# Performance work log

Measured on AMD Instinct MI355X. Metric: run time of the kernel, lower is better.

## Reference

```python
import jax, jax.numpy as jnp
import numpy as np

# ---- static hash-grid config (instant-NGP style, matches tcnn hash.json) ----
N_LEVELS = 16
F_PER_LEVEL = 2
LOG2_T = 19
TABLE_SIZE = 2 ** LOG2_T          # 524288 entries per level
BASE_RES = 16
PER_LEVEL_SCALE = 1.3819          # finest res ~2048
RES = [int(np.floor(BASE_RES * PER_LEVEL_SCALE ** l)) for l in range(N_LEVELS)]
N_POINTS = 2 ** 21
PRIME_Y = np.uint32(2654435761)   # tcnn spatial-hash prime

_CORNERS = jnp.array([[0, 0], [1, 0], [0, 1], [1, 1]], dtype=jnp.uint32)


def _level_features(x, table, res):
    """Bilinear hash-grid lookup for one level. x: [N,2] in [0,1). -> [N,F]."""
    pos = x * res                      # [N,2]
    x0f = jnp.floor(pos)
    w = pos - x0f                      # interpolation fractions [N,2]
    x0 = x0f.astype(jnp.uint32)
    c = x0[:, None, :] + _CORNERS[None]            # [N,4,2] corner coords
    if (res + 1) ** 2 <= TABLE_SIZE:
        # dense grid fits in the table: linear indexing (as tcnn does)
        idx = c[..., 0] + c[..., 1] * jnp.uint32(res + 1)
    else:
        # spatial hash with uint32 wraparound
        idx = (c[..., 0] ^ (c[..., 1] * PRIME_Y)) & jnp.uint32(TABLE_SIZE - 1)
    feats = table[idx.astype(jnp.int32)]           # [N,4,F] irregular gather
    wx = jnp.where(_CORNERS[None, :, 0] == 1, w[:, None, 0], 1.0 - w[:, None, 0])
    wy = jnp.where(_CORNERS[None, :, 1] == 1, w[:, None, 1], 1.0 - w[:, None, 1])
    return jnp.sum(feats * (wx * wy)[..., None], axis=1)  # [N,F]


def setup_inputs() -> dict:
    key = jax.random.key(0)
    k1, k2, k3, k4, k5 = jax.random.split(key, 5)
    x = jax.random.uniform(k1, (N_POINTS, 2), dtype=jnp.float32)
    # tcnn hash tables are initialized uniform in [-1e-4, 1e-4]
    tables = jax.random.uniform(k2, (N_LEVELS, TABLE_SIZE, F_PER_LEVEL),
                                dtype=jnp.float32, minval=-1e-4, maxval=1e-4)
    d_in = 2 + N_LEVELS * F_PER_LEVEL  # 34
    h = 64
    w1 = jax.random.normal(k3, (d_in, h), dtype=jnp.float32) * (1.0 / np.sqrt(d_in))
    w2 = jax.random.normal(k4, (h, h), dtype=jnp.float32) * (1.0 / np.sqrt(h))
    w3 = jax.random.normal(k5, (h, 3), dtype=jnp.float32) * (1.0 / np.sqrt(h))
    return {"x": x, "tables": tables, "w1": w1, "w2": w2, "w3": w3}


def reference(x, tables, w1, w2, w3):
    # multi-res hash grid encode (16 levels, static small loop)
    feats = [_level_features(x, tables[l], RES[l]) for l in range(N_LEVELS)]
    enc = jnp.concatenate([x] + feats, axis=1)     # [N, 2 + 32]
    # tiny fused MLP decode (no biases, as in tcnn networks)
    h = jax.nn.relu(enc @ w1)
    h = jax.nn.relu(h @ w2)
    return h @ w3                                   # [N, 3]
```

## Files before the change

### kernel.cpp

```cpp
#include <hip/hip_runtime.h>

typedef unsigned int u32;
typedef unsigned short u16;
typedef __attribute__((ext_vector_type(8))) short s16x8;
typedef __attribute__((ext_vector_type(4))) float f32x4;
typedef float f32x4a __attribute__((ext_vector_type(4), aligned(8)));
typedef u32  u32x2a  __attribute__((ext_vector_type(2), aligned(4)));

#define TBL    524288u
#define TMASK  (TBL - 1u)
#define HPRIME 2654435761u

__device__ constexpr int RESI[16] = {16,22,30,42,58,80,111,153,212,294,406,561,775,1072,1481,2047};

static __device__ __forceinline__ u16 f2bf(float f){
  u32 u = __builtin_bit_cast(u32, f);
  return (u16)((u + 0x7fffu + ((u >> 16) & 1u)) >> 16);
}
static __device__ __forceinline__ float bf2f(u16 h){ return __builtin_bit_cast(float, (u32)h << 16); }
static __device__ __forceinline__ float blo(u32 e){ return __builtin_bit_cast(float, (u32)(e << 16)); }
static __device__ __forceinline__ float bhi(u32 e){ return __builtin_bit_cast(float, (u32)(e & 0xffff0000u)); }
static __device__ __forceinline__ u32 packbf2(float a, float b){ return (u32)f2bf(a) | ((u32)f2bf(b) << 16); }
static __device__ __forceinline__ u32 cvtpk(float a, float b){
  u32 r; asm("v_cvt_pk_bf16_f32 %0, %1, %2" : "=v"(r) : "v"(a), "v"(b)); return r;
}

#define MFMA(A,B,C) __builtin_amdgcn_mfma_f32_16x16x32_bf16((A),(B),(C),0,0,0)

__global__ __launch_bounds__(256) void cvt_tab(const float4* __restrict__ src,
                                               uint2* __restrict__ dst, int n4) {
  for (int i = blockIdx.x*256 + threadIdx.x; i < n4; i += gridDim.x*256) {
    const float4 v = src[i];
    dst[i] = make_uint2(packbf2(v.x, v.y), packbf2(v.z, v.w));
  }
}

template<bool PACKED>
__global__ __launch_bounds__(256, 2) void ngp_fused(
    const float2* __restrict__ xq,
    const float2* __restrict__ tab32,
    const u32*    __restrict__ ctab,
    const float*  __restrict__ w1,
    const float*  __restrict__ w2,
    const float*  __restrict__ w3,
    float* __restrict__ out,
    int iters)
{
  __shared__ __align__(16) u16   encS[256 * 40];
  __shared__ __align__(16) float xyS [256 * 2];
  __shared__ __align__(16) u16   hS  [4][2][16*80];
  __shared__ __align__(16) s16x8 wS  [10][64];

  const int tid  = threadIdx.x;
  const int lane = tid & 63;
  const int wv   = tid >> 6;
  const int m    = lane & 15;
  const int q    = lane >> 4;

  float w1x[4], w1y[4];
  s16x8 B1[4], B2h[4][2], B3h[2];
  #pragma unroll
  for (int c = 0; c < 4; ++c) {
    const int n = c*16 + m;
    w1x[c] = w1[n]; w1y[c] = w1[64 + n];
    s16x8 f1;
    #pragma unroll
    for (int j = 0; j < 8; ++j) {
      const int k = q*8 + j;
      f1[j] = (short)f2bf(w1[(2 + k)*64 + n]);
    }
    B1[c] = f1;
    #pragma unroll
    for (int s = 0; s < 2; ++s) {
      s16x8 fh, fl;
      #pragma unroll
      for (int j = 0; j < 8; ++j) {
        const int k = s*32 + q*8 + j;
        const float v = w2[k*64 + n];
        const u16 h = f2bf(v);
        fh[j] = (short)h; fl[j] = (short)f2bf(v - bf2f(h));
      }
      B2h[c][s] = fh;
      if (wv == 0) wS[c*2 + s][lane] = fl;
    }
  }
  #pragma unroll
  for (int s = 0; s < 2; ++s) {
    s16x8 fh, fl;
    #pragma unroll
    for (int j = 0; j < 8; ++j) {
      const int k = s*32 + q*8 + j;
      const float v = (m < 3) ? w3[k*3 + m] : 0.f;
      const u16 h = f2bf(v);
      fh[j] = (short)h; fl[j] = (short)f2bf(v - bf2f(h));
    }
    B3h[s] = fh;
    if (wv == 0) wS[8 + s][lane] = fl;
  }
  __syncthreads();

  u16* const hpl = &hS[wv][0][0];
  u16* const lpl = &hS[wv][1][0];
  const int mq8  = (m & 12) << 1;

  for (int it = 0; it < iters; ++it) {
    const int base = (blockIdx.x * iters + it) << 8;

    {
      const float2 xy = xq[base + tid];
      ((float2*)xyS)[tid] = xy;
      const float xf = xy.x, yf = xy.y;
      u32 er[16];
      if constexpr (PACKED) {
        u32 hv[4][4];
        #pragma unroll
        for (int l = 12; l < 16; ++l) {
          const int res = RESI[l];
          const u32 ix = (u32)floorf(xf * (float)res);
          const u32 iy = (u32)floorf(yf * (float)res);
          const u32 hy = iy * HPRIME, hy1 = hy + HPRIME;
          const u32* t = ctab + (size_t)l * TBL;
          hv[l-12][0] = t[( ix       ^ hy ) & TMASK];
          hv[l-12][1] = t[((ix + 1u) ^ hy ) & TMASK];
          hv[l-12][2] = t[( ix       ^ hy1) & TMASK];
          hv[l-12][3] = t[((ix + 1u) ^ hy1) & TMASK];
        }
        #pragma unroll
        for (int l = 0; l < 12; ++l) {
          const int res = RESI[l];
          const float px = xf * (float)res, py = yf * (float)res;
          const float fx = floorf(px), fy = floorf(py);
          const float wx = px - fx, wy = py - fy;
          const u32 ix = (u32)fx, iy = (u32)fy;
          const float w00 = (1.f-wx)*(1.f-wy), w10 = wx*(1.f-wy);
          const float w01 = (1.f-wx)*wy,       w11 = wx*wy;
          const u32 st  = (u32)res + 1u;
          const u32 i00 = ix + iy*st;
          const u32* t = ctab + (size_t)l * TBL;
          const u32x2a eA = *(const u32x2a*)&t[i00];
          const u32x2a eB = *(const u32x2a*)&t[i00 + st];
          const float f0 = blo(eA[0])*w00 + blo(eA[1])*w10 + blo(eB[0])*w01 + blo(eB[1])*w11;
          const float f1 = bhi(eA[0])*w00 + bhi(eA[1])*w10 + bhi(eB[0])*w01 + bhi(eB[1])*w11;
          er[l] = cvtpk(f0, f1);
        }
        #pragma unroll
        for (int hl = 0; hl < 4; ++hl) {
          const int res = RESI[12 + hl];
          const float px = xf * (float)res, py = yf * (float)res;
          const float wx = px - floorf(px), wy = py - floorf(py);
          const float w00 = (1.f-wx)*(1.f-wy), w10 = wx*(1.f-wy);
          const float w01 = (1.f-wx)*wy,       w11 = wx*wy;
          const float f0 = blo(hv[hl][0])*w00 + blo(hv[hl][1])*w10
                         + blo(hv[hl][2])*w01 + blo(hv[hl][3])*w11;
          const float f1 = bhi(hv[hl][0])*w00 + bhi(hv[hl][1])*w10
                         + bhi(hv[hl][2])*w01 + bhi(hv[hl][3])*w11;
          er[12 + hl] = cvtpk(f0, f1);
        }
      } else {
        #pragma unroll
        for (int l = 0; l < 16; ++l) {
          const int res = RESI[l];
          const float px = xf * (float)res, py = yf * (float)res;
          const float fx = floorf(px), fy = floorf(py);
          const float wx = px - fx, wy = py - fy;
          const u32 ix = (u32)fx, iy = (u32)fy;
          const float w00 = (1.f-wx)*(1.f-wy), w10 = wx*(1.f-wy);
          const float w01 = (1.f-wx)*wy,       w11 = wx*wy;
          float f0, f1;
          if (l < 12) {
            const u32 st  = (u32)res + 1u;
            const u32 i00 = ix + iy*st;
            const float2* t = tab32 + (size_t)l * TBL;
            const f32x4a eA = *(const f32x4a*)&t[i00];
            const f32x4a eB = *(const f32x4a*)&t[i00 + st];
            f0 = eA[0]*w00 + eA[2]*w10 + eB[0]*w01 + eB[2]*w11;
            f1 = eA[1]*w00 + eA[3]*w10 + eB[1]*w01 + eB[3]*w11;
          } else {
            const u32 hy = iy * HPRIME, hy1 = hy + HPRIME;
            const u32 i00 = ( ix        ^ hy ) & TMASK;
            const u32 i10 = ((ix + 1u)  ^ hy ) & TMASK;
            const u32 i01 = ( ix        ^ hy1) & TMASK;
            const u32 i11 = ((ix + 1u)  ^ hy1) & TMASK;
            const float2* t = tab32 + (size_t)l * TBL;
            const float2 e00 = t[i00], e10 = t[i10], e01 = t[i01], e11 = t[i11];
            f0 = e00.x*w00 + e10.x*w10 + e01.x*w01 + e11.x*w11;
            f1 = e00.y*w00 + e10.y*w10 + e01.y*w01 + e11.y*w11;
          }
          er[l] = cvtpk(f0, f1);
        }
      }
      uint4* rowp = (uint4*)&encS[tid * 40];
      rowp[0] = make_uint4(er[0],  er[1],  er[2],  er[3]);
      rowp[1] = make_uint4(er[4],  er[5],  er[6],  er[7]);
      rowp[2] = make_uint4(er[8],  er[9],  er[10], er[11]);
      rowp[3] = make_uint4(er[12], er[13], er[14], er[15]);
    }

    #pragma unroll 1
    for (int t4 = 0; t4 < 4; ++t4) {
      const int rbase = wv*64 + t4*16;
      const s16x8 a1 = *(const s16x8*)&encS[(rbase + m)*40 + q*8];

      float xr[4], yr[4];
      #pragma unroll
      for (int r = 0; r < 4; ++r) {
        const float2 v = ((const float2*)xyS)[rbase + q*4 + r];
        xr[r] = v.x; yr[r] = v.y;
      }

      f32x4 acc[4];
      #pragma unroll
      for (int c = 0; c < 4; ++c) {
        f32x4 z;
        #pragma unroll
        for (int r = 0; r < 4; ++r) z[r] = xr[r]*w1x[c] + yr[r]*w1y[c];
        acc[c] = MFMA(a1, B1[c], z);
      }

      #pragma unroll
      for (int c = 0; c < 4; ++c)
        #pragma unroll
        for (int r = 0; r < 4; ++r) {
          const float h = fmaxf(acc[c][r], 0.f);
          const u32 hp_ = cvtpk(h, h);
          const float lf = h - __builtin_bit_cast(float, hp_ << 16);
          const u32 lp_ = cvtpk(lf, lf);
          const int idx = (q*4 + r)*80 + ((c*16 + m) ^ (q << 3));
          hpl[idx] = (u16)hp_;
          lpl[idx] = (u16)lp_;
        }

      s16x8 hi0 = *(const s16x8*)&hpl[m*80 + ((q*8) ^ mq8)];
      s16x8 hi1 = *(const s16x8*)&hpl[m*80 + 32 + ((q*8) ^ mq8)];
      s16x8 lo0 = *(const s16x8*)&lpl[m*80 + ((q*8) ^ mq8)];
      s16x8 lo1 = *(const s16x8*)&lpl[m*80 + 32 + ((q*8) ^ mq8)];

      #pragma unroll
      for (int c = 0; c < 4; ++c) {
        const s16x8 b2l0 = wS[c*2 + 0][lane];
        const s16x8 b2l1 = wS[c*2 + 1][lane];
        f32x4 z = {0.f,0.f,0.f,0.f};
        z = MFMA(hi0, B2h[c][0], z); z = MFMA(hi1, B2h[c][1], z);
        z = MFMA(lo0, B2h[c][0], z); z = MFMA(lo1, B2h[c][1], z);
        z = MFMA(hi0, b2l0,      z); z = MFMA(hi1, b2l1,      z);
        acc[c] = z;
      }

      #pragma unroll
      for (int c = 0; c < 4; ++c)
        #pragma unroll
        for (int r = 0; r < 4; ++r) {
          const float h = fmaxf(acc[c][r], 0.f);
          const u32 hp_ = cvtpk(h, h);
          const float lf = h - __builtin_bit_cast(float, hp_ << 16);
          const u32 lp_ = cvtpk(lf, lf);
          const int idx = (q*4 + r)*80 + ((c*16 + m) ^ (q << 3));
          hpl[idx] = (u16)hp_;
          lpl[idx] = (u16)lp_;
        }

      hi0 = *(const s16x8*)&hpl[m*80 + ((q*8) ^ mq8)];
      hi1 = *(const s16x8*)&hpl[m*80 + 32 + ((q*8) ^ mq8)];
      lo0 = *(const s16x8*)&lpl[m*80 + ((q*8) ^ mq8)];
      lo1 = *(const s16x8*)&lpl[m*80 + 32 + ((q*8) ^ mq8)];

      const s16x8 b3l0 = wS[8][lane];
      const s16x8 b3l1 = wS[9][lane];
      f32x4 z = {0.f,0.f,0.f,0.f};
      z = MFMA(hi0, B3h[0], z); z = MFMA(hi1, B3h[1], z);
      z = MFMA(lo0, B3h[0], z); z = MFMA(lo1, B3h[1], z);
      z = MFMA(hi0, b3l0,   z); z = MFMA(hi1, b3l1,   z);

      if (m < 3) {
        #pragma unroll
        for (int r = 0; r < 4; ++r)
          out[(size_t)(base + rbase + q*4 + r)*3 + m] = z[r];
      }
    }
  }
}

extern "C" void kernel_launch(void* const* d_in, const int* in_sizes, int n_in,
                              void* d_out, int out_size, void* d_ws, size_t ws_size,
                              hipStream_t stream) {
  const int N = in_sizes[0] / 2;
  const int ITERS = 4;
  const int blocks = N / (256 * ITERS);
  const size_t ctab_bytes = (size_t)16 * TBL * 4;
  if (ws_size >= ctab_bytes) {
    cvt_tab<<<2048, 256, 0, stream>>>((const float4*)d_in[1], (uint2*)d_ws, (int)(16*TBL/2));
    ngp_fused<true><<<blocks, 256, 0, stream>>>(
        (const float2*)d_in[0], (const float2*)d_in[1], (const u32*)d_ws,
        (const float*)d_in[2], (const float*)d_in[3], (const float*)d_in[4],
        (float*)d_out, ITERS);
  } else {
    ngp_fused<false><<<blocks, 256, 0, stream>>>(
        (const float2*)d_in[0], (const float2*)d_in[1], (const u32*)d_ws,
        (const float*)d_in[2], (const float*)d_in[3], (const float*)d_in[4],
        (float*)d_out, ITERS);
  }
}
```

Before: 433.7 us.

## Sort points by Morton key before hash-grid lookup and scatter outputs

Adds a counting sort of input points into a 256x256 Morton-ordered bin layout (histogram, scan, scatter kernels), so the fused encoder+MLP kernel processes spatially coherent points and its table gathers get better cache locality. Outputs are written back through a permutation array. It also changes the LDS hidden-activation layout from an XOR-swizzled 80-stride to a plain 72-stride padding. The cost is extra kernels with global atomics, a single-block scan, and extra workspace and memory traffic, and the new padding may change bank conflicts.

```diff
diff --git a/kernel.cpp b/kernel.cpp
--- a/kernel.cpp
+++ b/kernel.cpp
@@ -10,6 +10,7 @@
 #define TBL    524288u
 #define TMASK  (TBL - 1u)
 #define HPRIME 2654435761u
+#define NBINS  65536
 
 __device__ constexpr int RESI[16] = {16,22,30,42,58,80,111,153,212,294,406,561,775,1072,1481,2047};
 
@@ -24,6 +25,18 @@
 static __device__ __forceinline__ u32 cvtpk(float a, float b){
   u32 r; asm("v_cvt_pk_bf16_f32 %0, %1, %2" : "=v"(r) : "v"(a), "v"(b)); return r;
 }
+static __device__ __forceinline__ u32 spread8(u32 v){
+  v &= 0xFFu;
+  v = (v | (v << 4)) & 0x0F0Fu;
+  v = (v | (v << 2)) & 0x3333u;
+  v = (v | (v << 1)) & 0x5555u;
+  return v;
+}
+static __device__ __forceinline__ u32 mkey(float x, float y){
+  u32 kx = (u32)(x * 256.f); kx = kx > 255u ? 255u : kx;
+  u32 ky = (u32)(y * 256.f); ky = ky > 255u ? 255u : ky;
+  return spread8(kx) | (spread8(ky) << 1);
+}
 
 #define MFMA(A,B,C) __builtin_amdgcn_mfma_f32_16x16x32_bf16((A),(B),(C),0,0,0)
 
@@ -35,11 +48,51 @@
   }
 }
 
-template<bool PACKED>
+__global__ __launch_bounds__(256) void hist_k(const float2* __restrict__ xq,
+                                              u32* __restrict__ hist, int n) {
+  for (int i = blockIdx.x*256 + threadIdx.x; i < n; i += gridDim.x*256) {
+    const float2 p = xq[i];
+    atomicAdd(&hist[mkey(p.x, p.y)], 1u);
+  }
+}
+__global__ __launch_bounds__(1024) void scan_k(u32* __restrict__ hist) {
+  __shared__ u32 part[1024];
+  const int t = threadIdx.x;
+  u32 s = 0;
+  for (int i = 0; i < 64; ++i) s += hist[t*64 + i];
+  part[t] = s;
+  __syncthreads();
+  for (int d = 1; d < 1024; d <<= 1) {
+    const u32 v = (t >= d) ? part[t - d] : 0u;
+    __syncthreads();
+    part[t] += v;
+    __syncthreads();
+  }
+  u32 run = part[t] - s;
+  for (int i = 0; i < 64; ++i) {
+    const u32 h = hist[t*64 + i];
+    hist[t*64 + i] = run;
+    run += h;
+  }
+}
+__global__ __launch_bounds__(256) void scat_k(const float2* __restrict__ xq,
+                                              u32* __restrict__ offs,
+                                              float2* __restrict__ xs,
+                                              u32* __restrict__ perm, int n) {
+  for (int i = blockIdx.x*256 + threadIdx.x; i < n; i += gridDim.x*256) {
+    const float2 p = xq[i];
+    const u32 pos = atomicAdd(&offs[mkey(p.x, p.y)], 1u);
+    xs[pos] = p;
+    perm[pos] = (u32)i;
+  }
+}
+
+template<bool PACKED, bool SORT>
 __global__ __launch_bounds__(256, 2) void ngp_fused(
     const float2* __restrict__ xq,
     const float2* __restrict__ tab32,
     const u32*    __restrict__ ctab,
+    const u32*    __restrict__ perm,
     const float*  __restrict__ w1,
     const float*  __restrict__ w2,
     const float*  __restrict__ w3,
@@ -48,7 +101,7 @@
 {
   __shared__ __align__(16) u16   encS[256 * 40];
   __shared__ __align__(16) float xyS [256 * 2];
-  __shared__ __align__(16) u16   hS  [4][2][16*80];
+  __shared__ __align__(16) u16   hS  [4][2][16*72];
   __shared__ __align__(16) s16x8 wS  [10][64];
 
   const int tid  = threadIdx.x;
@@ -101,7 +154,6 @@
 
   u16* const hpl = &hS[wv][0][0];
   u16* const lpl = &hS[wv][1][0];
-  const int mq8  = (m & 12) << 1;
 
   for (int it = 0; it < iters; ++it) {
     const int base = (blockIdx.x * iters + it) << 8;
@@ -225,15 +277,15 @@
           const u32 hp_ = cvtpk(h, h);
           const float lf = h - __builtin_bit_cast(float, hp_ << 16);
           const u32 lp_ = cvtpk(lf, lf);
-          const int idx = (q*4 + r)*80 + ((c*16 + m) ^ (q << 3));
+          const int idx = (q*4 + r)*72 + c*16 + m;
           hpl[idx] = (u16)hp_;
           lpl[idx] = (u16)lp_;
         }
 
-      s16x8 hi0 = *(const s16x8*)&hpl[m*80 + ((q*8) ^ mq8)];
-      s16x8 hi1 = *(const s16x8*)&hpl[m*80 + 32 + ((q*8) ^ mq8)];
-      s16x8 lo0 = *(const s16x8*)&lpl[m*80 + ((q*8) ^ mq8)];
-      s16x8 lo1 = *(const s16x8*)&lpl[m*80 + 32 + ((q*8) ^ mq8)];
+      s16x8 hi0 = *(const s16x8*)&hpl[m*72 + q*8];
+      s16x8 hi1 = *(const s16x8*)&hpl[m*72 + 32 + q*8];
+      s16x8 lo0 = *(const s16x8*)&lpl[m*72 + q*8];
+      s16x8 lo1 = *(const s16x8*)&lpl[m*72 + 32 + q*8];
 
       #pragma unroll
       for (int c = 0; c < 4; ++c) {
@@ -254,15 +306,15 @@
           const u32 hp_ = cvtpk(h, h);
           const float lf = h - __builtin_bit_cast(float, hp_ << 16);
           const u32 lp_ = cvtpk(lf, lf);
-          const int idx = (q*4 + r)*80 + ((c*16 + m) ^ (q << 3));
+          const int idx = (q*4 + r)*72 + c*16 + m;
           hpl[idx] = (u16)hp_;
           lpl[idx] = (u16)lp_;
         }
 
-      hi0 = *(const s16x8*)&hpl[m*80 + ((q*8) ^ mq8)];
-      hi1 = *(const s16x8*)&hpl[m*80 + 32 + ((q*8) ^ mq8)];
-      lo0 = *(const s16x8*)&lpl[m*80 + ((q*8) ^ mq8)];
-      lo1 = *(const s16x8*)&lpl[m*80 + 32 + ((q*8) ^ mq8)];
+      hi0 = *(const s16x8*)&hpl[m*72 + q*8];
+      hi1 = *(const s16x8*)&hpl[m*72 + 32 + q*8];
+      lo0 = *(const s16x8*)&lpl[m*72 + q*8];
+      lo1 = *(const s16x8*)&lpl[m*72 + 32 + q*8];
 
       const s16x8 b3l0 = wS[8][lane];
       const s16x8 b3l1 = wS[9][lane];
@@ -273,8 +325,11 @@
 
       if (m < 3) {
         #pragma unroll
-        for (int r = 0; r < 4; ++r)
-          out[(size_t)(base + rbase + q*4 + r)*3 + m] = z[r];
+        for (int r = 0; r < 4; ++r) {
+          const int pi = base + rbase + q*4 + r;
+          const size_t oi = SORT ? (size_t)perm[pi] : (size_t)pi;
+          out[oi*3 + m] = z[r];
+        }
       }
     }
   }
@@ -286,16 +341,35 @@
   const int N = in_sizes[0] / 2;
   const int ITERS = 4;
   const int blocks = N / (256 * ITERS);
-  const size_t ctab_bytes = (size_t)16 * TBL * 4;
-  if (ws_size >= ctab_bytes) {
+  const size_t ctab_b = (size_t)16 * TBL * 4;
+  const size_t xs_off  = ctab_b;
+  const size_t perm_off = xs_off + (size_t)N * 8;
+  const size_t hist_off = perm_off + (size_t)N * 4;
+  const size_t sort_need = hist_off + (size_t)NBINS * 4;
+
+  char* ws = (char*)d_ws;
+  if (ws_size >= sort_need) {
     cvt_tab<<<2048, 256, 0, stream>>>((const float4*)d_in[1], (uint2*)d_ws, (int)(16*TBL/2));
-    ngp_fused<true><<<blocks, 256, 0, stream>>>(
-        (const float2*)d_in[0], (const float2*)d_in[1], (const u32*)d_ws,
+    u32* hist = (u32*)(ws + hist_off);
+    float2* xs = (float2*)(ws + xs_off);
+    u32* perm  = (u32*)(ws + perm_off);
+    hipMemsetAsync(hist, 0, (size_t)NBINS * 4, stream);
+    hist_k<<<2048, 256, 0, stream>>>((const float2*)d_in[0], hist, N);
+    scan_k<<<1, 1024, 0, stream>>>(hist);
+    scat_k<<<2048, 256, 0, stream>>>((const float2*)d_in[0], hist, xs, perm, N);
+    ngp_fused<true, true><<<blocks, 256, 0, stream>>>(
+        xs, (const float2*)d_in[1], (const u32*)d_ws, perm,
+        (const float*)d_in[2], (const float*)d_in[3], (const float*)d_in[4],
+        (float*)d_out, ITERS);
+  } else if (ws_size >= ctab_b) {
+    cvt_tab<<<2048, 256, 0, stream>>>((const float4*)d_in[1], (uint2*)d_ws, (int)(16*TBL/2));
+    ngp_fused<true, false><<<blocks, 256, 0, stream>>>(
+        (const float2*)d_in[0], (const float2*)d_in[1], (const u32*)d_ws, nullptr,
         (const float*)d_in[2], (const float*)d_in[3], (const float*)d_in[4],
         (float*)d_out, ITERS);
   } else {
-    ngp_fused<false><<<blocks, 256, 0, stream>>>(
-        (const float2*)d_in[0], (const float2*)d_in[1], (const u32*)d_ws,
+    ngp_fused<false, false><<<blocks, 256, 0, stream>>>(
+        (const float2*)d_in[0], (const float2*)d_in[1], (const u32*)d_ws, nullptr,
         (const float*)d_in[2], (const float*)d_in[3], (const float*)d_in[4],
         (float*)d_out, ITERS);
   }
```

Measured after the change: 535.0 us. 1.23x slower.
